# Kernel tuning notes

Hardware: AMD Instinct MI355X
Metric: run time of the kernel (lower is better)

The kernel has to match this reference:

```python
import jax, jax.numpy as jnp
import numpy as np

N_PTS = 8192   # collocation points (original used 50; scaled up)
N_PARA = 5000  # rows of para, matching the source script
HID = 50


def setup_inputs() -> dict:
    key = jax.random.key(0)
    ks = jax.random.split(key, 10)
    x = jax.random.normal(ks[0], (N_PTS, 3), jnp.float32)
    # para = cat(normal(-2,1) [P,2], normal(0.5,1) [P,1]) as in source script
    a_b = jax.random.normal(ks[1], (N_PARA, 2), jnp.float32) * 1.0 - 2.0
    c = jax.random.normal(ks[2], (N_PARA, 1), jnp.float32) * 1.0 + 0.5
    para = jnp.concatenate([a_b, c], axis=1)

    def init(k, fan_in, shape):
        bound = 1.0 / np.sqrt(fan_in)  # torch Linear default init range
        return jax.random.uniform(k, shape, jnp.float32, -bound, bound)

    W_in = init(ks[3], 3, (3, HID))
    b_in = init(ks[4], 3, (HID,))
    W_hid = init(ks[5], HID, (4, HID, HID))
    b_hid = init(ks[6], HID, (4, HID))
    W_out = init(ks[7], HID, (HID, 2))
    b_out = init(ks[8], HID, (2,))
    return dict(x=x, para=para, W_in=W_in, b_in=b_in, W_hid=W_hid,
                b_hid=b_hid, W_out=W_out, b_out=b_out)


def reference(x, para, W_in, b_in, W_hid, b_hid, W_out, b_out):
    def net(xi):  # xi: [3] -> [2] (u, v)
        h = jnp.tanh(xi @ W_in + b_in)
        for i in range(W_hid.shape[0]):
            h = jnp.tanh(h @ W_hid[i] + b_hid[i])
        return h @ W_out + b_out

    uv = jax.vmap(net)(x)                    # [N, 2]
    jac = jax.vmap(jax.jacrev(net))(x)       # [N, 2, 3]
    hess = jax.vmap(jax.hessian(net))(x)     # [N, 2, 3, 3]

    u, v = uv[:, 0], uv[:, 1]
    u_t, v_t = jac[:, 0, 2], jac[:, 1, 2]
    u_xx, u_yy = hess[:, 0, 0, 0], hess[:, 0, 1, 1]
    v_xx, v_yy = hess[:, 1, 0, 0], hess[:, 1, 1, 1]

    Q = u * u + v * v  # |q|^2
    # f_2 = u_t + 0.5 v_xx + 0.5 a v_yy - 0.5 u_yy + Q v - Q c u + u
    # f_1 = v_t - 0.5 u_xx - 0.5 a u_yy - 0.5 v_yy - Q u - Q c v + v
    base2 = u_t + 0.5 * v_xx - 0.5 * u_yy + Q * v + u   # a,c-independent part
    base1 = v_t - 0.5 * u_xx - 0.5 * v_yy - Q * u + v

    a = para[:, 0:1]   # [P, 1]; column 1 (b) is unused, as in source
    cc = para[:, 2:3]

    f1 = base1[None, :] - 0.5 * a * u_yy[None, :] - cc * (Q * v)[None, :]  # [P, N]
    f2 = base2[None, :] + 0.5 * a * v_yy[None, :] - cc * (Q * u)[None, :]

    # per-row loss: MSE(f1, 0) + MSE(f2, 0)
    return jnp.mean(f1 * f1, axis=1) + jnp.mean(f2 * f2, axis=1)  # [P]
```

## Files before the change

### kernel.cpp

```cpp
#include <hip/hip_runtime.h>
#include <math.h>

#define HID 50
#define NPTS 8192
#define NPARA 5000
#define NLAYERS 4

typedef float f32x4 __attribute__((ext_vector_type(4)));
typedef short short8 __attribute__((ext_vector_type(8)));

union U4S8 { uint4 u; short8 s; };

#define WS_PART 0
#define WS_FRAG 32768
#define WS_WIN  98304
#define WS_BIN  99072
#define WS_BH   99328
#define WS_WOUT 100352
#define WS_NEED 100864

#define S_STRIDE 21
#define S_COMP   (64*S_STRIDE)
#define S_WORDS  (6*S_COMP)

#define SEL_HI 0x05040100u
#define SEL_LO 0x07060302u

__device__ __forceinline__ float fast_tanh(float x) {
    const float ax = __builtin_fabsf(x);
    const float e  = __expf(2.0f * ax);
    const float r  = __builtin_amdgcn_rcpf(e + 1.0f);
    const float t  = fmaf(-2.0f, r, 1.0f);
    return __builtin_copysignf(t, x);
}

__device__ __forceinline__ void split_bf16(float x, unsigned &hi, unsigned &lo) {
    const unsigned u = __float_as_uint(x);
    const unsigned h = u & 0xFFFF0000u;
    const float rem  = x - __uint_as_float(h);
    const unsigned r = __float_as_uint(rem);
    hi = h >> 16;
    lo = (r + 0x7FFFu + ((r >> 16) & 1u)) >> 16;
}

__device__ __forceinline__ unsigned pack_split(float x) {
    unsigned hi, lo;
    split_bf16(x, hi, lo);
    return hi | (lo << 16);
}

__device__ __forceinline__ float unpack_sum(unsigned w) {
    return __uint_as_float(w << 16) + __uint_as_float(w & 0xFFFF0000u);
}

__device__ __forceinline__ uint4 pack8(const unsigned v[8]) {
    return make_uint4(v[0] | (v[1] << 16), v[2] | (v[3] << 16),
                      v[4] | (v[5] << 16), v[6] | (v[7] << 16));
}

__global__ __launch_bounds__(256) void prep_kernel(
    const float* __restrict__ W_in, const float* __restrict__ b_in,
    const float* __restrict__ W_hid, const float* __restrict__ b_hid,
    const float* __restrict__ W_out, char* __restrict__ wsbase)
{
    const int gid = blockIdx.x * 256 + threadIdx.x;
    if (gid < 2048) {
        const int fid = gid >> 6, lane = gid & 63;
        const int l = fid >> 3, c = (fid >> 2) & 1, t = fid & 3;
        const int q = lane >> 4, n = lane & 15;
        const int gn = t*16 + n;
        unsigned hi[8], lo[8];
        #pragma unroll
        for (int jj = 0; jj < 8; ++jj) {
            const int k = c*32 + q*8 + jj;
            const float w = (k < HID && gn < HID) ? W_hid[(l*HID + k)*HID + gn] : 0.f;
            split_bf16(w, hi[jj], lo[jj]);
        }
        uint4* frag = (uint4*)(wsbase + WS_FRAG);
        frag[(fid*2 + 0)*64 + lane] = pack8(hi);
        frag[(fid*2 + 1)*64 + lane] = pack8(lo);
    } else if (gid < 2240) {
        const int i = gid - 2048, d = i >> 6, j = i & 63;
        ((float*)(wsbase + WS_WIN))[i] = (j < HID) ? W_in[d*HID + j] : 0.f;
    } else if (gid < 2304) {
        const int j = gid - 2240;
        ((float*)(wsbase + WS_BIN))[j] = (j < HID) ? b_in[j] : 0.f;
    } else if (gid < 2560) {
        const int i = gid - 2304, l = i >> 6, j = i & 63;
        ((float*)(wsbase + WS_BH))[i] = (j < HID) ? b_hid[l*HID + j] : 0.f;
    } else if (gid < 2688) {
        const int i = gid - 2560, j = i >> 1, s = i & 1;
        ((float*)(wsbase + WS_WOUT))[i] = (j < HID) ? W_out[j*2 + s] : 0.f;
    }
}

__global__ __launch_bounds__(128, 1) void point_mfma_kernel(
    const float* __restrict__ x,
    const float* __restrict__ b_out,
    const char* __restrict__ wsbase,
    double* __restrict__ part)
{
    __shared__ unsigned S[S_WORDS];
    __shared__ float xd[16][8];

    const int tid  = threadIdx.x;
    const int wave = tid >> 6;
    const int lane = tid & 63;
    const int q = lane >> 4, L = lane & 15;

    const float* Winp = (const float*)(wsbase + WS_WIN);
    const float* binp = (const float*)(wsbase + WS_BIN);
    const float* bhp  = (const float*)(wsbase + WS_BH);
    const float* wop  = (const float*)(wsbase + WS_WOUT);
    const uint4* frag = (const uint4*)(wsbase + WS_FRAG);

    const int pid = blockIdx.x * 16 + L;
    const float x0 = x[3*pid+0], x1 = x[3*pid+1], x2 = x[3*pid+2];
    #pragma unroll
    for (int jj = 0; jj < 8; ++jj) {
        const int j = 32*wave + 8*q + jj;
        const float w0 = Winp[j], w1 = Winp[64 + j], w2 = Winp[128 + j];
        const float z  = fmaf(x0, w0, fmaf(x1, w1, fmaf(x2, w2, binp[j])));
        const float h  = fast_tanh(z);
        const float s  = 1.f - h*h;
        const float g  = -2.f*h*s;
        const int base = j*S_STRIDE + L;
        S[0*S_COMP + base] = pack_split(h);
        S[1*S_COMP + base] = pack_split(s*w0);
        S[2*S_COMP + base] = pack_split(s*w1);
        S[3*S_COMP + base] = pack_split(s*w2);
        S[4*S_COMP + base] = pack_split(g*w0*w0);
        S[5*S_COMP + base] = pack_split(g*w1*w1);
    }
    __syncthreads();

    #pragma unroll 1
    for (int l = 0; l < NLAYERS; ++l) {
        uint4 Bh[2][2], Bl[2][2];
        #pragma unroll
        for (int c = 0; c < 2; ++c)
            #pragma unroll
            for (int tt = 0; tt < 2; ++tt) {
                const int fi = (l*2 + c)*4 + (2*wave + tt);
                Bh[c][tt] = frag[(fi*2 + 0)*64 + lane];
                Bl[c][tt] = frag[(fi*2 + 1)*64 + lane];
            }

        uint4 Ah[2][6], Al[2][6];
        #pragma unroll
        for (int c = 0; c < 2; ++c)
            #pragma unroll
            for (int comp = 0; comp < 6; ++comp) {
                const int base = comp*S_COMP + (c*32 + q*8)*S_STRIDE + L;
                unsigned w[8];
                #pragma unroll
                for (int jj = 0; jj < 8; ++jj) w[jj] = S[base + jj*S_STRIDE];
                Ah[c][comp] = make_uint4(
                    __builtin_amdgcn_perm(w[1], w[0], SEL_HI),
                    __builtin_amdgcn_perm(w[3], w[2], SEL_HI),
                    __builtin_amdgcn_perm(w[5], w[4], SEL_HI),
                    __builtin_amdgcn_perm(w[7], w[6], SEL_HI));
                Al[c][comp] = make_uint4(
                    __builtin_amdgcn_perm(w[1], w[0], SEL_LO),
                    __builtin_amdgcn_perm(w[3], w[2], SEL_LO),
                    __builtin_amdgcn_perm(w[5], w[4], SEL_LO),
                    __builtin_amdgcn_perm(w[7], w[6], SEL_LO));
            }
        __syncthreads();

        f32x4 acc[6][2];
        #pragma unroll
        for (int comp = 0; comp < 6; ++comp)
            #pragma unroll
            for (int tt = 0; tt < 2; ++tt)
                acc[comp][tt] = (f32x4){0.f, 0.f, 0.f, 0.f};

        #pragma unroll
        for (int c = 0; c < 2; ++c)
            #pragma unroll
            for (int comp = 0; comp < 6; ++comp) {
                U4S8 ah, al; ah.u = Ah[c][comp]; al.u = Al[c][comp];
                #pragma unroll
                for (int tt = 0; tt < 2; ++tt) {
                    U4S8 bh, bl; bh.u = Bh[c][tt]; bl.u = Bl[c][tt];
                    acc[comp][tt] = __builtin_amdgcn_mfma_f32_16x16x32_bf16(ah.s, bh.s, acc[comp][tt], 0, 0, 0);
                    acc[comp][tt] = __builtin_amdgcn_mfma_f32_16x16x32_bf16(ah.s, bl.s, acc[comp][tt], 0, 0, 0);
                    acc[comp][tt] = __builtin_amdgcn_mfma_f32_16x16x32_bf16(al.s, bh.s, acc[comp][tt], 0, 0, 0);
                }
            }

        #pragma unroll
        for (int tt = 0; tt < 2; ++tt) {
            const int j = (2*wave + tt)*16 + L;
            const float bias = bhp[l*64 + j];
            #pragma unroll
            for (int r = 0; r < 4; ++r) {
                const int p = 4*q + r;
                const float za  = acc[0][tt][r] + bias;
                const float zx  = acc[1][tt][r];
                const float zy  = acc[2][tt][r];
                const float zt  = acc[3][tt][r];
                const float zxx = acc[4][tt][r];
                const float zyy = acc[5][tt][r];
                const float h = fast_tanh(za);
                const float s = 1.f - h*h;
                const float g = -2.f*h*s;
                const int base = j*S_STRIDE + p;
                S[0*S_COMP + base] = pack_split(h);
                S[1*S_COMP + base] = pack_split(s*zx);
                S[2*S_COMP + base] = pack_split(s*zy);
                S[3*S_COMP + base] = pack_split(s*zt);
                S[4*S_COMP + base] = pack_split(fmaf(g*zx, zx, s*zxx));
                S[5*S_COMP + base] = pack_split(fmaf(g*zy, zy, s*zyy));
            }
        }
        __syncthreads();
    }

    float du=0.f, dv=0.f, dut=0.f, dvt=0.f, duxx=0.f, dvxx=0.f, duyy=0.f, dvyy=0.f;
    #pragma unroll
    for (int jj = 0; jj < 8; ++jj) {
        const int j = 32*wave + 8*q + jj;
        const int base = j*S_STRIDE + L;
        const float sh  = unpack_sum(S[0*S_COMP + base]);
        const float st_ = unpack_sum(S[3*S_COMP + base]);
        const float sxx = unpack_sum(S[4*S_COMP + base]);
        const float syy = unpack_sum(S[5*S_COMP + base]);
        const float w0 = wop[j*2 + 0], w1 = wop[j*2 + 1];
        du   = fmaf(sh,  w0, du);   dv   = fmaf(sh,  w1, dv);
        dut  = fmaf(st_, w0, dut);  dvt  = fmaf(st_, w1, dvt);
        duxx = fmaf(sxx, w0, duxx); dvxx = fmaf(sxx, w1, dvxx);
        duyy = fmaf(syy, w0, duyy); dvyy = fmaf(syy, w1, dvyy);
    }
    #pragma unroll
    for (int off = 16; off <= 32; off <<= 1) {
        du   += __shfl_xor(du,   off); dv   += __shfl_xor(dv,   off);
        dut  += __shfl_xor(dut,  off); dvt  += __shfl_xor(dvt,  off);
        duxx += __shfl_xor(duxx, off); dvxx += __shfl_xor(dvxx, off);
        duyy += __shfl_xor(duyy, off); dvyy += __shfl_xor(dvyy, off);
    }
    if (wave == 1 && lane < 16) {
        xd[lane][0]=du;   xd[lane][1]=dv;   xd[lane][2]=dut;  xd[lane][3]=dvt;
        xd[lane][4]=duxx; xd[lane][5]=dvxx; xd[lane][6]=duyy; xd[lane][7]=dvyy;
    }
    __syncthreads();
    if (wave == 0) {
        du   += xd[L][0]; dv   += xd[L][1]; dut  += xd[L][2]; dvt  += xd[L][3];
        duxx += xd[L][4]; dvxx += xd[L][5]; duyy += xd[L][6]; dvyy += xd[L][7];

        const float u = du + b_out[0];
        const float v = dv + b_out[1];
        const float Q = u*u + v*v;
        const float g1 = dvt - 0.5f*duxx - 0.5f*dvyy - Q*u + v;
        const float g2 = dut + 0.5f*dvxx - 0.5f*duyy + Q*v + u;
        const float h1 = 0.5f*duyy, h2 = 0.5f*dvyy;
        const float k1 = Q*v,       k2 = Q*u;

        const double m = (lane < 16) ? 1.0 : 0.0;
        double a0 = m * ((double)g1*(double)g1 + (double)g2*(double)g2);
        double a1 = m * ((double)h1*(double)h1 + (double)h2*(double)h2);
        double a2 = m * ((double)k1*(double)k1 + (double)k2*(double)k2);
        double a3 = m * ((double)g2*(double)h2 - (double)g1*(double)h1);
        double a4 = m * ((double)g1*(double)k1 + (double)g2*(double)k2);
        double a5 = m * ((double)h1*(double)k1 - (double)h2*(double)k2);
        #pragma unroll
        for (int off = 1; off <= 32; off <<= 1) {
            a0 += __shfl_xor(a0, off); a1 += __shfl_xor(a1, off);
            a2 += __shfl_xor(a2, off); a3 += __shfl_xor(a3, off);
            a4 += __shfl_xor(a4, off); a5 += __shfl_xor(a5, off);
        }
        if (lane == 0) {
            double* o = &part[blockIdx.x * 6];
            o[0] = a0; o[1] = a1; o[2] = a2; o[3] = a3; o[4] = a4; o[5] = a5;
        }
    }
}

#define BLOCK_F 1024
#define WPB_F   16
#define GRID_F  512
#define SWIN_SZ (3*HID + 16)
#define SBIN_SZ (HID + 16)
#define SWH_SZ  (NLAYERS*HID*HID + 16)
#define SBH_SZ  (NLAYERS*HID + 16)
#define SWO_SZ  (2*64)

__device__ __forceinline__ float readlane_f(float v, int k) {
    return __int_as_float(__builtin_amdgcn_readlane(__float_as_int(v), k));
}

__global__ __launch_bounds__(BLOCK_F, 8) void point_fallback_kernel(
    const float* __restrict__ x,
    const float* __restrict__ W_in, const float* __restrict__ b_in,
    const float* __restrict__ W_hid, const float* __restrict__ b_hid,
    const float* __restrict__ W_out, const float* __restrict__ b_out,
    double* __restrict__ part, int use_atomic)
{
    __shared__ float sWin[SWIN_SZ];
    __shared__ float sbin[SBIN_SZ];
    __shared__ float sWh[SWH_SZ];
    __shared__ float sbh[SBH_SZ];
    __shared__ float sWo[SWO_SZ];
    __shared__ float sbo[2];
    __shared__ double sRed[WPB_F][6];

    const int tid = threadIdx.x;
    for (int i = tid; i < 3*HID; i += BLOCK_F) sWin[i] = W_in[i];
    for (int i = 3*HID + tid; i < SWIN_SZ; i += BLOCK_F) sWin[i] = 0.f;
    for (int i = tid; i < HID; i += BLOCK_F) sbin[i] = b_in[i];
    for (int i = HID + tid; i < SBIN_SZ; i += BLOCK_F) sbin[i] = 0.f;
    for (int i = tid; i < NLAYERS*HID*HID; i += BLOCK_F) sWh[i] = W_hid[i];
    for (int i = NLAYERS*HID*HID + tid; i < SWH_SZ; i += BLOCK_F) sWh[i] = 0.f;
    for (int i = tid; i < NLAYERS*HID; i += BLOCK_F) sbh[i] = b_hid[i];
    for (int i = NLAYERS*HID + tid; i < SBH_SZ; i += BLOCK_F) sbh[i] = 0.f;
    for (int i = tid; i < 2*HID; i += BLOCK_F) sWo[i] = W_out[i];
    for (int i = 2*HID + tid; i < SWO_SZ; i += BLOCK_F) sWo[i] = 0.f;
    if (tid < 2) sbo[tid] = b_out[tid];
    __syncthreads();

    const int lane = tid & 63;
    const int wave = tid >> 6;
    const int p    = blockIdx.x * WPB_F + wave;

    const float x0 = x[3*p+0], x1 = x[3*p+1], x2 = x[3*p+2];
    const float w0 = sWin[lane];
    const float w1 = sWin[HID + lane];
    const float w2 = sWin[2*HID + lane];
    float z = fmaf(x0, w0, fmaf(x1, w1, fmaf(x2, w2, sbin[lane])));
    float h = fast_tanh(z);
    float s = 1.f - h*h;
    float hx = s*w0, hy = s*w1, ht = s*w2;
    float hxx = -2.f*h*s*w0*w0;
    float hyy = -2.f*h*s*w1*w1;

    for (int l = 0; l < NLAYERS; ++l) {
        const float* __restrict__ Wl = &sWh[l*HID*HID];
        float za  = sbh[l*HID + lane];
        float zx = 0.f, zy = 0.f, zt = 0.f, zxx = 0.f, zyy = 0.f;
        #pragma unroll
        for (int k = 0; k < HID; ++k) {
            const float w = Wl[k*HID + lane];
            za  = fmaf(readlane_f(h,   k), w, za);
            zx  = fmaf(readlane_f(hx,  k), w, zx);
            zy  = fmaf(readlane_f(hy,  k), w, zy);
            zt  = fmaf(readlane_f(ht,  k), w, zt);
            zxx = fmaf(readlane_f(hxx, k), w, zxx);
            zyy = fmaf(readlane_f(hyy, k), w, zyy);
        }
        const float hn = fast_tanh(za);
        const float sn = 1.f - hn*hn;
        hxx = fmaf(sn, zxx, -2.f*hn*sn*zx*zx);
        hyy = fmaf(sn, zyy, -2.f*hn*sn*zy*zy);
        hx = sn*zx; hy = sn*zy; ht = sn*zt;
        h = hn;
    }

    const float wo0 = sWo[lane*2+0];
    const float wo1 = sWo[lane*2+1];
    const bool act = (lane < HID);
    float pu   = act ? h  *wo0 : 0.f;
    float pv   = act ? h  *wo1 : 0.f;
    float put  = act ? ht *wo0 : 0.f;
    float pvt  = act ? ht *wo1 : 0.f;
    float puxx = act ? hxx*wo0 : 0.f;
    float pvxx = act ? hxx*wo1 : 0.f;
    float puyy = act ? hyy*wo0 : 0.f;
    float pvyy = act ? hyy*wo1 : 0.f;
    #pragma unroll
    for (int off = 32; off > 0; off >>= 1) {
        pu   += __shfl_xor(pu,   off);
        pv   += __shfl_xor(pv,   off);
        put  += __shfl_xor(put,  off);
        pvt  += __shfl_xor(pvt,  off);
        puxx += __shfl_xor(puxx, off);
        pvxx += __shfl_xor(pvxx, off);
        puyy += __shfl_xor(puyy, off);
        pvyy += __shfl_xor(pvyy, off);
    }
    const float u = pu + sbo[0];
    const float v = pv + sbo[1];
    const float Q = u*u + v*v;
    const float g1 = pvt - 0.5f*puxx - 0.5f*pvyy - Q*u + v;
    const float g2 = put + 0.5f*pvxx - 0.5f*puyy + Q*v + u;
    const float h1 = 0.5f*puyy, h2 = 0.5f*pvyy;
    const float k1 = Q*v,       k2 = Q*u;

    const double a0 = (double)g1*(double)g1 + (double)g2*(double)g2;
    const double a1 = (double)h1*(double)h1 + (double)h2*(double)h2;
    const double a2 = (double)k1*(double)k1 + (double)k2*(double)k2;
    const double a3 = (double)g2*(double)h2 - (double)g1*(double)h1;
    const double a4 = (double)g1*(double)k1 + (double)g2*(double)k2;
    const double a5 = (double)h1*(double)k1 - (double)h2*(double)k2;

    if (lane == 0) {
        sRed[wave][0] = a0; sRed[wave][1] = a1; sRed[wave][2] = a2;
        sRed[wave][3] = a3; sRed[wave][4] = a4; sRed[wave][5] = a5;
    }
    __syncthreads();
    if (tid < 6) {
        double t = 0.0;
        #pragma unroll
        for (int wv = 0; wv < WPB_F; ++wv) t += sRed[wv][tid];
        if (use_atomic) atomicAdd(&part[tid], t);
        else            part[blockIdx.x * 6 + tid] = t;
    }
}

__global__ __launch_bounds__(512) void para_kernel(
    const float* __restrict__ para,
    const double* __restrict__ part, int nsets,
    float* __restrict__ out)
{
    __shared__ double sW[8][6];
    __shared__ double sS[6];
    const int tid  = threadIdx.x;
    const int lane = tid & 63;
    const int wave = tid >> 6;

    double c0=0,c1=0,c2=0,c3=0,c4=0,c5=0;
    for (int i = tid; i < nsets; i += 512) {
        const double* qp = &part[i*6];
        c0 += qp[0]; c1 += qp[1]; c2 += qp[2]; c3 += qp[3]; c4 += qp[4]; c5 += qp[5];
    }
    #pragma unroll
    for (int off = 32; off > 0; off >>= 1) {
        c0 += __shfl_xor(c0, off); c1 += __shfl_xor(c1, off);
        c2 += __shfl_xor(c2, off); c3 += __shfl_xor(c3, off);
        c4 += __shfl_xor(c4, off); c5 += __shfl_xor(c5, off);
    }
    if (lane == 0) {
        sW[wave][0]=c0; sW[wave][1]=c1; sW[wave][2]=c2;
        sW[wave][3]=c3; sW[wave][4]=c4; sW[wave][5]=c5;
    }
    __syncthreads();
    if (tid < 6) {
        double t = 0.0;
        #pragma unroll
        for (int wv = 0; wv < 8; ++wv) t += sW[wv][tid];
        sS[tid] = t;
    }
    __syncthreads();

    const double S0=sS[0], S1=sS[1], S2=sS[2], S3=sS[3], S4=sS[4], S5=sS[5];
    for (int p = blockIdx.x * 512 + tid; p < NPARA; p += gridDim.x * 512) {
        const double a  = (double)para[3*p+0];
        const double cc = (double)para[3*p+2];
        const double r = S0 + a*a*S1 + cc*cc*S2 + 2.0*a*S3 - 2.0*cc*S4 + 2.0*a*cc*S5;
        out[p] = (float)(r * (1.0 / (double)NPTS));
    }
}

extern "C" void kernel_launch(void* const* d_in, const int* in_sizes, int n_in,
                              void* d_out, int out_size, void* d_ws, size_t ws_size,
                              hipStream_t stream) {
    const float* x     = (const float*)d_in[0];
    const float* para  = (const float*)d_in[1];
    const float* W_in  = (const float*)d_in[2];
    const float* b_in  = (const float*)d_in[3];
    const float* W_hid = (const float*)d_in[4];
    const float* b_hid = (const float*)d_in[5];
    const float* W_out = (const float*)d_in[6];
    const float* b_out = (const float*)d_in[7];

    char*   wsbase = (char*)d_ws;
    double* part   = (double*)d_ws;

    if (ws_size >= (size_t)WS_NEED) {
        prep_kernel<<<11, 256, 0, stream>>>(W_in, b_in, W_hid, b_hid, W_out, wsbase);
        point_mfma_kernel<<<512, 128, 0, stream>>>(x, b_out, wsbase, part);
        para_kernel<<<10, 512, 0, stream>>>(para, part, 512, (float*)d_out);
    } else if (ws_size >= (size_t)(GRID_F * 6 * sizeof(double))) {
        point_fallback_kernel<<<GRID_F, BLOCK_F, 0, stream>>>(
            x, W_in, b_in, W_hid, b_hid, W_out, b_out, part, 0);
        para_kernel<<<10, 512, 0, stream>>>(para, part, GRID_F, (float*)d_out);
    } else {
        hipMemsetAsync(part, 0, 6*sizeof(double), stream);
        point_fallback_kernel<<<GRID_F, BLOCK_F, 0, stream>>>(
            x, W_in, b_in, W_hid, b_hid, W_out, b_out, part, 1);
        para_kernel<<<10, 512, 0, stream>>>(para, part, 1, (float*)d_out);
    }
}
```

Baseline: 89.02 us.

## Transpose LDS staging layout for vector access and fuse para reduction via last-block

The shared-memory activation buffer moves from a j-major strided layout to a point-major layout with a padded row stride, so A-fragment loads and output-layer reads become 128-bit vector LDS accesses instead of eight scalar loads. The para_kernel launch is also removed: each block publishes its partial sums, bumps an atomic counter, and the last block reduces all partials and writes the 5000 outputs. This saves one kernel launch and many LDS instructions. In exchange the whole final stage runs serially on a single 128-thread block, and the scattered per-point stores in the epilogue may now hit bank conflicts.

```diff
diff --git a/kernel.cpp b/kernel.cpp
--- a/kernel.cpp
+++ b/kernel.cpp
@@ -5,6 +5,7 @@
 #define NPTS 8192
 #define NPARA 5000
 #define NLAYERS 4
+#define NBLK 512
 
 typedef float f32x4 __attribute__((ext_vector_type(4)));
 typedef short short8 __attribute__((ext_vector_type(8)));
@@ -17,11 +18,12 @@
 #define WS_BIN  99072
 #define WS_BH   99328
 #define WS_WOUT 100352
-#define WS_NEED 100864
-
-#define S_STRIDE 21
-#define S_COMP   (64*S_STRIDE)
-#define S_WORDS  (6*S_COMP)
+#define WS_CNT  100864
+#define WS_NEED 100992
+
+#define KS      68
+#define S_COMP  (16*KS)
+#define S_WORDS (6*S_COMP)
 
 #define SEL_HI 0x05040100u
 #define SEL_LO 0x07060302u
@@ -91,17 +93,22 @@
     } else if (gid < 2688) {
         const int i = gid - 2560, j = i >> 1, s = i & 1;
         ((float*)(wsbase + WS_WOUT))[i] = (j < HID) ? W_out[j*2 + s] : 0.f;
+    } else if (gid == 2688) {
+        *(unsigned*)(wsbase + WS_CNT) = 0u;
     }
 }
 
 __global__ __launch_bounds__(128, 1) void point_mfma_kernel(
     const float* __restrict__ x,
     const float* __restrict__ b_out,
-    const char* __restrict__ wsbase,
-    double* __restrict__ part)
+    const float* __restrict__ para,
+    char* __restrict__ wsbase,
+    double* __restrict__ part,
+    float* __restrict__ out)
 {
-    __shared__ unsigned S[S_WORDS];
+    __shared__ __align__(16) unsigned S[S_WORDS];
     __shared__ float xd[16][8];
+    __shared__ unsigned sLast;
 
     const int tid  = threadIdx.x;
     const int wave = tid >> 6;
@@ -117,20 +124,28 @@
     const int pid = blockIdx.x * 16 + L;
     const float x0 = x[3*pid+0], x1 = x[3*pid+1], x2 = x[3*pid+2];
     #pragma unroll
-    for (int jj = 0; jj < 8; ++jj) {
-        const int j = 32*wave + 8*q + jj;
-        const float w0 = Winp[j], w1 = Winp[64 + j], w2 = Winp[128 + j];
-        const float z  = fmaf(x0, w0, fmaf(x1, w1, fmaf(x2, w2, binp[j])));
-        const float h  = fast_tanh(z);
-        const float s  = 1.f - h*h;
-        const float g  = -2.f*h*s;
-        const int base = j*S_STRIDE + L;
-        S[0*S_COMP + base] = pack_split(h);
-        S[1*S_COMP + base] = pack_split(s*w0);
-        S[2*S_COMP + base] = pack_split(s*w1);
-        S[3*S_COMP + base] = pack_split(s*w2);
-        S[4*S_COMP + base] = pack_split(g*w0*w0);
-        S[5*S_COMP + base] = pack_split(g*w1*w1);
+    for (int half = 0; half < 2; ++half) {
+        unsigned pk[6][4];
+        #pragma unroll
+        for (int jj = 0; jj < 4; ++jj) {
+            const int j = 32*wave + 8*q + half*4 + jj;
+            const float w0 = Winp[j], w1 = Winp[64 + j], w2 = Winp[128 + j];
+            const float z  = fmaf(x0, w0, fmaf(x1, w1, fmaf(x2, w2, binp[j])));
+            const float h  = fast_tanh(z);
+            const float s  = 1.f - h*h;
+            const float g  = -2.f*h*s;
+            pk[0][jj] = pack_split(h);
+            pk[1][jj] = pack_split(s*w0);
+            pk[2][jj] = pack_split(s*w1);
+            pk[3][jj] = pack_split(s*w2);
+            pk[4][jj] = pack_split(g*w0*w0);
+            pk[5][jj] = pack_split(g*w1*w1);
+        }
+        #pragma unroll
+        for (int comp = 0; comp < 6; ++comp) {
+            uint4* dst = (uint4*)&S[comp*S_COMP + L*KS + 32*wave + 8*q + half*4];
+            *dst = make_uint4(pk[comp][0], pk[comp][1], pk[comp][2], pk[comp][3]);
+        }
     }
     __syncthreads();
 
@@ -151,20 +166,19 @@
         for (int c = 0; c < 2; ++c)
             #pragma unroll
             for (int comp = 0; comp < 6; ++comp) {
-                const int base = comp*S_COMP + (c*32 + q*8)*S_STRIDE + L;
-                unsigned w[8];
-                #pragma unroll
-                for (int jj = 0; jj < 8; ++jj) w[jj] = S[base + jj*S_STRIDE];
+                const uint4* src = (const uint4*)&S[comp*S_COMP + L*KS + c*32 + q*8];
+                const uint4 wA = src[0];
+                const uint4 wB = src[1];
                 Ah[c][comp] = make_uint4(
-                    __builtin_amdgcn_perm(w[1], w[0], SEL_HI),
-                    __builtin_amdgcn_perm(w[3], w[2], SEL_HI),
-                    __builtin_amdgcn_perm(w[5], w[4], SEL_HI),
-                    __builtin_amdgcn_perm(w[7], w[6], SEL_HI));
+                    __builtin_amdgcn_perm(wA.y, wA.x, SEL_HI),
+                    __builtin_amdgcn_perm(wA.w, wA.z, SEL_HI),
+                    __builtin_amdgcn_perm(wB.y, wB.x, SEL_HI),
+                    __builtin_amdgcn_perm(wB.w, wB.z, SEL_HI));
                 Al[c][comp] = make_uint4(
-                    __builtin_amdgcn_perm(w[1], w[0], SEL_LO),
-                    __builtin_amdgcn_perm(w[3], w[2], SEL_LO),
-                    __builtin_amdgcn_perm(w[5], w[4], SEL_LO),
-                    __builtin_amdgcn_perm(w[7], w[6], SEL_LO));
+                    __builtin_amdgcn_perm(wA.y, wA.x, SEL_LO),
+                    __builtin_amdgcn_perm(wA.w, wA.z, SEL_LO),
+                    __builtin_amdgcn_perm(wB.y, wB.x, SEL_LO),
+                    __builtin_amdgcn_perm(wB.w, wB.z, SEL_LO));
             }
         __syncthreads();
 
@@ -205,7 +219,7 @@
                 const float h = fast_tanh(za);
                 const float s = 1.f - h*h;
                 const float g = -2.f*h*s;
-                const int base = j*S_STRIDE + p;
+                const int base = p*KS + j;
                 S[0*S_COMP + base] = pack_split(h);
                 S[1*S_COMP + base] = pack_split(s*zx);
                 S[2*S_COMP + base] = pack_split(s*zy);
@@ -218,19 +232,35 @@
     }
 
     float du=0.f, dv=0.f, dut=0.f, dvt=0.f, duxx=0.f, dvxx=0.f, duyy=0.f, dvyy=0.f;
-    #pragma unroll
-    for (int jj = 0; jj < 8; ++jj) {
-        const int j = 32*wave + 8*q + jj;
-        const int base = j*S_STRIDE + L;
-        const float sh  = unpack_sum(S[0*S_COMP + base]);
-        const float st_ = unpack_sum(S[3*S_COMP + base]);
-        const float sxx = unpack_sum(S[4*S_COMP + base]);
-        const float syy = unpack_sum(S[5*S_COMP + base]);
-        const float w0 = wop[j*2 + 0], w1 = wop[j*2 + 1];
-        du   = fmaf(sh,  w0, du);   dv   = fmaf(sh,  w1, dv);
-        dut  = fmaf(st_, w0, dut);  dvt  = fmaf(st_, w1, dvt);
-        duxx = fmaf(sxx, w0, duxx); dvxx = fmaf(sxx, w1, dvxx);
-        duyy = fmaf(syy, w0, duyy); dvyy = fmaf(syy, w1, dvyy);
+    {
+        const int jb = 32*wave + 8*q;
+        const uint4* s0 = (const uint4*)&S[0*S_COMP + L*KS + jb];
+        const uint4* s3 = (const uint4*)&S[3*S_COMP + L*KS + jb];
+        const uint4* s4 = (const uint4*)&S[4*S_COMP + L*KS + jb];
+        const uint4* s5 = (const uint4*)&S[5*S_COMP + L*KS + jb];
+        uint4 h0 = s0[0], h1 = s0[1];
+        uint4 t0 = s3[0], t1 = s3[1];
+        uint4 xx0 = s4[0], xx1 = s4[1];
+        uint4 yy0 = s5[0], yy1 = s5[1];
+        const unsigned* hw = (const unsigned*)&h0;
+        unsigned ha[8] = {h0.x,h0.y,h0.z,h0.w,h1.x,h1.y,h1.z,h1.w};
+        unsigned ta[8] = {t0.x,t0.y,t0.z,t0.w,t1.x,t1.y,t1.z,t1.w};
+        unsigned xa[8] = {xx0.x,xx0.y,xx0.z,xx0.w,xx1.x,xx1.y,xx1.z,xx1.w};
+        unsigned ya[8] = {yy0.x,yy0.y,yy0.z,yy0.w,yy1.x,yy1.y,yy1.z,yy1.w};
+        (void)hw;
+        #pragma unroll
+        for (int jj = 0; jj < 8; ++jj) {
+            const int j = jb + jj;
+            const float w0 = wop[j*2 + 0], w1 = wop[j*2 + 1];
+            const float sh  = unpack_sum(ha[jj]);
+            const float st_ = unpack_sum(ta[jj]);
+            const float sxx = unpack_sum(xa[jj]);
+            const float syy = unpack_sum(ya[jj]);
+            du   = fmaf(sh,  w0, du);   dv   = fmaf(sh,  w1, dv);
+            dut  = fmaf(st_, w0, dut);  dvt  = fmaf(st_, w1, dvt);
+            duxx = fmaf(sxx, w0, duxx); dvxx = fmaf(sxx, w1, dvxx);
+            duyy = fmaf(syy, w0, duyy); dvyy = fmaf(syy, w1, dvyy);
+        }
     }
     #pragma unroll
     for (int off = 16; off <= 32; off <<= 1) {
@@ -271,7 +301,54 @@
         }
         if (lane == 0) {
             double* o = &part[blockIdx.x * 6];
-            o[0] = a0; o[1] = a1; o[2] = a2; o[3] = a3; o[4] = a4; o[5] = a5;
+            #pragma unroll
+            for (int i = 0; i < 6; ++i) {
+                const double vv = (i==0)?a0:(i==1)?a1:(i==2)?a2:(i==3)?a3:(i==4)?a4:a5;
+                __hip_atomic_store(&o[i], vv, __ATOMIC_RELAXED, __HIP_MEMORY_SCOPE_AGENT);
+            }
+            __threadfence();
+            unsigned* cnt = (unsigned*)(wsbase + WS_CNT);
+            const unsigned vv = __hip_atomic_fetch_add(cnt, 1u, __ATOMIC_ACQ_REL,
+                                                       __HIP_MEMORY_SCOPE_AGENT);
+            sLast = (vv == (unsigned)(NBLK - 1)) ? 1u : 0u;
+        }
+    }
+    __syncthreads();
+
+    if (sLast) {
+        __threadfence();
+        double c0=0,c1=0,c2=0,c3=0,c4=0,c5=0;
+        for (int i = tid; i < NBLK; i += 128) {
+            const double* qp = &part[i*6];
+            c0 += __hip_atomic_load(&qp[0], __ATOMIC_RELAXED, __HIP_MEMORY_SCOPE_AGENT);
+            c1 += __hip_atomic_load(&qp[1], __ATOMIC_RELAXED, __HIP_MEMORY_SCOPE_AGENT);
+            c2 += __hip_atomic_load(&qp[2], __ATOMIC_RELAXED, __HIP_MEMORY_SCOPE_AGENT);
+            c3 += __hip_atomic_load(&qp[3], __ATOMIC_RELAXED, __HIP_MEMORY_SCOPE_AGENT);
+            c4 += __hip_atomic_load(&qp[4], __ATOMIC_RELAXED, __HIP_MEMORY_SCOPE_AGENT);
+            c5 += __hip_atomic_load(&qp[5], __ATOMIC_RELAXED, __HIP_MEMORY_SCOPE_AGENT);
+        }
+        #pragma unroll
+        for (int off = 1; off <= 32; off <<= 1) {
+            c0 += __shfl_xor(c0, off); c1 += __shfl_xor(c1, off);
+            c2 += __shfl_xor(c2, off); c3 += __shfl_xor(c3, off);
+            c4 += __shfl_xor(c4, off); c5 += __shfl_xor(c5, off);
+        }
+        __shared__ double sW2[2][6];
+        __shared__ double sS2[6];
+        if (lane == 0) {
+            sW2[wave][0]=c0; sW2[wave][1]=c1; sW2[wave][2]=c2;
+            sW2[wave][3]=c3; sW2[wave][4]=c4; sW2[wave][5]=c5;
+        }
+        __syncthreads();
+        if (tid < 6) sS2[tid] = sW2[0][tid] + sW2[1][tid];
+        __syncthreads();
+        const double S0=sS2[0], S1=sS2[1], S2=sS2[2],
+                     S3=sS2[3], S4=sS2[4], S5=sS2[5];
+        for (int p = tid; p < NPARA; p += 128) {
+            const double a  = (double)para[3*p+0];
+            const double cc = (double)para[3*p+2];
+            const double r = S0 + a*a*S1 + cc*cc*S2 + 2.0*a*S3 - 2.0*cc*S4 + 2.0*a*cc*S5;
+            out[p] = (float)(r * (1.0 / (double)NPTS));
         }
     }
 }
@@ -467,8 +544,8 @@
 
     if (ws_size >= (size_t)WS_NEED) {
         prep_kernel<<<11, 256, 0, stream>>>(W_in, b_in, W_hid, b_hid, W_out, wsbase);
-        point_mfma_kernel<<<512, 128, 0, stream>>>(x, b_out, wsbase, part);
-        para_kernel<<<10, 512, 0, stream>>>(para, part, 512, (float*)d_out);
+        point_mfma_kernel<<<NBLK, 128, 0, stream>>>(x, b_out, para, wsbase, part,
+                                                    (float*)d_out);
     } else if (ws_size >= (size_t)(GRID_F * 6 * sizeof(double))) {
         point_fallback_kernel<<<GRID_F, BLOCK_F, 0, stream>>>(
             x, W_in, b_in, W_hid, b_hid, W_out, b_out, part, 0);
```

Result: slower. 109.1 us (+22.6%).

## Split point MLP block across four waves, one 16-column output tile each

Applied to the files above, without the earlier changes.

The per-point MLP kernel now uses 256 threads (four waves) per block instead of two, with each wave owning one 16-wide hidden-unit tile instead of two. MFMA accumulators and fragment loads shrink per wave, and the A fragments are consumed immediately rather than buffered across the whole layer, cutting register pressure and allowing two blocks per CU. The cost is that each wave redundantly reads the full shared-memory activation tile, and the final reduction now combines partials from three extra waves.

```diff
diff --git a/kernel.cpp b/kernel.cpp
--- a/kernel.cpp
+++ b/kernel.cpp
@@ -5,6 +5,7 @@
 #define NPTS 8192
 #define NPARA 5000
 #define NLAYERS 4
+#define NBLK 512
 
 typedef float f32x4 __attribute__((ext_vector_type(4)));
 typedef short short8 __attribute__((ext_vector_type(8)));
@@ -94,14 +95,14 @@
     }
 }
 
-__global__ __launch_bounds__(128, 1) void point_mfma_kernel(
+__global__ __launch_bounds__(256, 2) void point_mfma_kernel(
     const float* __restrict__ x,
     const float* __restrict__ b_out,
     const char* __restrict__ wsbase,
     double* __restrict__ part)
 {
     __shared__ unsigned S[S_WORDS];
-    __shared__ float xd[16][8];
+    __shared__ float xd[3][16][8];
 
     const int tid  = threadIdx.x;
     const int wave = tid >> 6;
@@ -117,8 +118,8 @@
     const int pid = blockIdx.x * 16 + L;
     const float x0 = x[3*pid+0], x1 = x[3*pid+1], x2 = x[3*pid+2];
     #pragma unroll
-    for (int jj = 0; jj < 8; ++jj) {
-        const int j = 32*wave + 8*q + jj;
+    for (int jj = 0; jj < 4; ++jj) {
+        const int j = 16*wave + 4*q + jj;
         const float w0 = Winp[j], w1 = Winp[64 + j], w2 = Winp[128 + j];
         const float z  = fmaf(x0, w0, fmaf(x1, w1, fmaf(x2, w2, binp[j])));
         const float h  = fast_tanh(z);
@@ -136,72 +137,54 @@
 
     #pragma unroll 1
     for (int l = 0; l < NLAYERS; ++l) {
-        uint4 Bh[2][2], Bl[2][2];
-        #pragma unroll
-        for (int c = 0; c < 2; ++c)
-            #pragma unroll
-            for (int tt = 0; tt < 2; ++tt) {
-                const int fi = (l*2 + c)*4 + (2*wave + tt);
-                Bh[c][tt] = frag[(fi*2 + 0)*64 + lane];
-                Bl[c][tt] = frag[(fi*2 + 1)*64 + lane];
+        f32x4 acc[6];
+        #pragma unroll
+        for (int comp = 0; comp < 6; ++comp) acc[comp] = (f32x4){0.f,0.f,0.f,0.f};
+
+        #pragma unroll
+        for (int c = 0; c < 2; ++c) {
+            U4S8 bh, bl;
+            {
+                const int fi = (l*2 + c)*4 + wave;
+                bh.u = frag[(fi*2 + 0)*64 + lane];
+                bl.u = frag[(fi*2 + 1)*64 + lane];
             }
-
-        uint4 Ah[2][6], Al[2][6];
-        #pragma unroll
-        for (int c = 0; c < 2; ++c)
             #pragma unroll
             for (int comp = 0; comp < 6; ++comp) {
                 const int base = comp*S_COMP + (c*32 + q*8)*S_STRIDE + L;
                 unsigned w[8];
                 #pragma unroll
                 for (int jj = 0; jj < 8; ++jj) w[jj] = S[base + jj*S_STRIDE];
-                Ah[c][comp] = make_uint4(
+                U4S8 ah, al;
+                ah.u = make_uint4(
                     __builtin_amdgcn_perm(w[1], w[0], SEL_HI),
                     __builtin_amdgcn_perm(w[3], w[2], SEL_HI),
                     __builtin_amdgcn_perm(w[5], w[4], SEL_HI),
                     __builtin_amdgcn_perm(w[7], w[6], SEL_HI));
-                Al[c][comp] = make_uint4(
+                al.u = make_uint4(
                     __builtin_amdgcn_perm(w[1], w[0], SEL_LO),
                     __builtin_amdgcn_perm(w[3], w[2], SEL_LO),
                     __builtin_amdgcn_perm(w[5], w[4], SEL_LO),
                     __builtin_amdgcn_perm(w[7], w[6], SEL_LO));
+                acc[comp] = __builtin_amdgcn_mfma_f32_16x16x32_bf16(ah.s, bh.s, acc[comp], 0, 0, 0);
+                acc[comp] = __builtin_amdgcn_mfma_f32_16x16x32_bf16(ah.s, bl.s, acc[comp], 0, 0, 0);
+                acc[comp] = __builtin_amdgcn_mfma_f32_16x16x32_bf16(al.s, bh.s, acc[comp], 0, 0, 0);
             }
+        }
         __syncthreads();
 
-        f32x4 acc[6][2];
-        #pragma unroll
-        for (int comp = 0; comp < 6; ++comp)
-            #pragma unroll
-            for (int tt = 0; tt < 2; ++tt)
-                acc[comp][tt] = (f32x4){0.f, 0.f, 0.f, 0.f};
-
-        #pragma unroll
-        for (int c = 0; c < 2; ++c)
-            #pragma unroll
-            for (int comp = 0; comp < 6; ++comp) {
-                U4S8 ah, al; ah.u = Ah[c][comp]; al.u = Al[c][comp];
-                #pragma unroll
-                for (int tt = 0; tt < 2; ++tt) {
-                    U4S8 bh, bl; bh.u = Bh[c][tt]; bl.u = Bl[c][tt];
-                    acc[comp][tt] = __builtin_amdgcn_mfma_f32_16x16x32_bf16(ah.s, bh.s, acc[comp][tt], 0, 0, 0);
-                    acc[comp][tt] = __builtin_amdgcn_mfma_f32_16x16x32_bf16(ah.s, bl.s, acc[comp][tt], 0, 0, 0);
-                    acc[comp][tt] = __builtin_amdgcn_mfma_f32_16x16x32_bf16(al.s, bh.s, acc[comp][tt], 0, 0, 0);
-                }
-            }
-
-        #pragma unroll
-        for (int tt = 0; tt < 2; ++tt) {
-            const int j = (2*wave + tt)*16 + L;
+        {
+            const int j = wave*16 + L;
             const float bias = bhp[l*64 + j];
             #pragma unroll
             for (int r = 0; r < 4; ++r) {
                 const int p = 4*q + r;
-                const float za  = acc[0][tt][r] + bias;
-                const float zx  = acc[1][tt][r];
-                const float zy  = acc[2][tt][r];
-                const float zt  = acc[3][tt][r];
-                const float zxx = acc[4][tt][r];
-                const float zyy = acc[5][tt][r];
+                const float za  = acc[0][r] + bias;
+                const float zx  = acc[1][r];
+                const float zy  = acc[2][r];
+                const float zt  = acc[3][r];
+                const float zxx = acc[4][r];
+                const float zyy = acc[5][r];
                 const float h = fast_tanh(za);
                 const float s = 1.f - h*h;
                 const float g = -2.f*h*s;
@@ -219,8 +202,8 @@
 
     float du=0.f, dv=0.f, dut=0.f, dvt=0.f, duxx=0.f, dvxx=0.f, duyy=0.f, dvyy=0.f;
     #pragma unroll
-    for (int jj = 0; jj < 8; ++jj) {
-        const int j = 32*wave + 8*q + jj;
+    for (int jj = 0; jj < 4; ++jj) {
+        const int j = 16*wave + 4*q + jj;
         const int base = j*S_STRIDE + L;
         const float sh  = unpack_sum(S[0*S_COMP + base]);
         const float st_ = unpack_sum(S[3*S_COMP + base]);
@@ -239,15 +222,19 @@
         duxx += __shfl_xor(duxx, off); dvxx += __shfl_xor(dvxx, off);
         duyy += __shfl_xor(duyy, off); dvyy += __shfl_xor(dvyy, off);
     }
-    if (wave == 1 && lane < 16) {
-        xd[lane][0]=du;   xd[lane][1]=dv;   xd[lane][2]=dut;  xd[lane][3]=dvt;
-        xd[lane][4]=duxx; xd[lane][5]=dvxx; xd[lane][6]=duyy; xd[lane][7]=dvyy;
+    if (wave >= 1 && lane < 16) {
+        float* d = xd[wave-1][lane];
+        d[0]=du; d[1]=dv; d[2]=dut; d[3]=dvt;
+        d[4]=duxx; d[5]=dvxx; d[6]=duyy; d[7]=dvyy;
     }
     __syncthreads();
     if (wave == 0) {
-        du   += xd[L][0]; dv   += xd[L][1]; dut  += xd[L][2]; dvt  += xd[L][3];
-        duxx += xd[L][4]; dvxx += xd[L][5]; duyy += xd[L][6]; dvyy += xd[L][7];
-
+        #pragma unroll
+        for (int wv = 0; wv < 3; ++wv) {
+            const float* d = xd[wv][L];
+            du += d[0]; dv += d[1]; dut += d[2]; dvt += d[3];
+            duxx += d[4]; dvxx += d[5]; duyy += d[6]; dvyy += d[7];
+        }
         const float u = du + b_out[0];
         const float v = dv + b_out[1];
         const float Q = u*u + v*v;
@@ -467,8 +454,8 @@
 
     if (ws_size >= (size_t)WS_NEED) {
         prep_kernel<<<11, 256, 0, stream>>>(W_in, b_in, W_hid, b_hid, W_out, wsbase);
-        point_mfma_kernel<<<512, 128, 0, stream>>>(x, b_out, wsbase, part);
-        para_kernel<<<10, 512, 0, stream>>>(para, part, 512, (float*)d_out);
+        point_mfma_kernel<<<NBLK, 256, 0, stream>>>(x, b_out, wsbase, part);
+        para_kernel<<<10, 512, 0, stream>>>(para, part, NBLK, (float*)d_out);
     } else if (ws_size >= (size_t)(GRID_F * 6 * sizeof(double))) {
         point_fallback_kernel<<<GRID_F, BLOCK_F, 0, stream>>>(
             x, W_in, b_in, W_hid, b_hid, W_out, b_out, part, 0);
```

Result: faster. 86.46 us (median of 2 runs) (-2.9%).
